# Optimization experiments

Hardware: AMD Instinct MI355X
Metric: run time of the kernel (lower is better)

## Reference

```python
import jax, jax.numpy as jnp
import numpy as np

B, N, C, H = 2, 2048, 1024, 16
D = C // H  # head_dim = 64

def setup_inputs() -> dict:
    key = jax.random.key(0)
    ks = jax.random.split(key, 8)
    x = jax.random.normal(ks[0], (B, N, C), jnp.float32)
    mask = jax.random.uniform(ks[1], (H, N, N), jnp.float32)
    gamma = jax.random.uniform(ks[2], (H,), jnp.float32)  # per-head decay in (0,1)
    state_prev = jax.random.normal(ks[3], (B, H, D, D), jnp.float32)
    w_scale = 0.02
    W_qkv = jax.random.normal(ks[4], (C, 3 * C), jnp.float32) * w_scale
    b_qkv = jnp.zeros((3 * C,), jnp.float32)
    W_out = jax.random.normal(ks[5], (C, C), jnp.float32) * w_scale
    b_out = jnp.zeros((C,), jnp.float32)
    return dict(x=x, mask=mask, gamma=gamma, state_prev=state_prev,
                W_qkv=W_qkv, b_qkv=b_qkv, W_out=W_out, b_out=b_out)

def reference(x, mask, gamma, state_prev, W_qkv, b_qkv, W_out, b_out):
    # Retention.chunkwise with state_prev (mode='chunkwise')
    b, n, c = x.shape
    h = gamma.shape[0]
    d = c // h
    scale = d ** -0.5
    qkv = (x @ W_qkv + b_qkv).reshape(b, n, 3, h, d)
    q = qkv[:, :, 0].transpose(0, 2, 1, 3) * scale  # [B,H,N,D]
    k = qkv[:, :, 1].transpose(0, 2, 1, 3)
    v = qkv[:, :, 2].transpose(0, 2, 1, 3)
    # intra-chunk decay-masked retention: [B,H,N,N]
    ret = jnp.einsum('bhnd,bhmd->bhnm', q, k) * mask
    ret = jnp.einsum('bhnm,bhmd->bhnd', ret, v)  # [B,H,N,D]
    inner_pos = jnp.arange(1, n + 1, dtype=x.dtype)  # [N], 1-based positions
    # state = sum_n gamma^(N-n) * k_n^T v_n (no [B,H,N,D,D] materialization)
    state_decays = gamma[:, None] ** (n - inner_pos)[None, :]  # [H,N]
    state = jnp.einsum('bhnd,bhne,hn->bhde', k, v, state_decays)  # [B,H,D,D]
    chunk_decay = gamma ** n  # [H]
    state = state + state_prev * chunk_decay[None, :, None, None]
    # cross-chunk retention against previous state
    cross = jnp.einsum('bhnd,bhde->bhne', q, state_prev)
    cross = cross * (gamma[None, :, None, None] ** inner_pos[None, None, :, None])
    ret = (ret + cross).transpose(0, 2, 1, 3).reshape(b, n, c)
    out = ret @ W_out + b_out
    return (out, state)
```

## Files before the change

kernel.cpp:

```cpp
#include <hip/hip_runtime.h>
#include <hip/hip_bf16.h>
#include <cstdint>

#define DI __device__ __forceinline__

typedef __attribute__((ext_vector_type(8))) short v8s;
typedef __attribute__((ext_vector_type(4))) float v4f;

constexpr int Bc = 2, Nc = 2048, Cc = 1024, Hc = 16, Dc = 64;

DI float bfbits(uint32_t u) { union { uint32_t i; float f; } c; c.i = u; return c.f; }
DI unsigned short f2bf(float f) {
    union { float f; uint32_t u; } c; c.f = f;
    uint32_t r = c.u + 0x7FFFu + ((c.u >> 16) & 1u);
    return (unsigned short)(r >> 16);
}
DI void unpackb8(uint4 u, float* f) {
    f[0] = bfbits(u.x << 16); f[1] = bfbits(u.x & 0xFFFF0000u);
    f[2] = bfbits(u.y << 16); f[3] = bfbits(u.y & 0xFFFF0000u);
    f[4] = bfbits(u.z << 16); f[5] = bfbits(u.z & 0xFFFF0000u);
    f[6] = bfbits(u.w << 16); f[7] = bfbits(u.w & 0xFFFF0000u);
}
DI float gpow(float g, float p) {
    if (p <= 0.f) return 1.f;
    if (g <= 0.f) return 0.f;
    return exp2f(p * log2f(g));
}

__global__ __launch_bounds__(256) void cvt_bf16(
    const float* __restrict__ in, unsigned short* __restrict__ out, int n8)
{
    int i = blockIdx.x * 256 + threadIdx.x;
    if (i >= n8) return;
    float4 a = ((const float4*)in)[i * 2];
    float4 b = ((const float4*)in)[i * 2 + 1];
    ushort4 r0; r0.x = f2bf(a.x); r0.y = f2bf(a.y); r0.z = f2bf(a.z); r0.w = f2bf(a.w);
    ushort4 r1; r1.x = f2bf(b.x); r1.y = f2bf(b.y); r1.z = f2bf(b.z); r1.w = f2bf(b.w);
    ((ushort4*)out)[i * 2] = r0; ((ushort4*)out)[i * 2 + 1] = r1;
}

__global__ __launch_bounds__(256) void transpose_cvt(
    const float* __restrict__ in, unsigned short* __restrict__ out, int R, int C)
{
    __shared__ float T[64][65];
    const int tid = threadIdx.x;
    const int r0 = blockIdx.y * 64, c0 = blockIdx.x * 64;
    #pragma unroll
    for (int rep = 0; rep < 4; rep++) {
        int row = (tid >> 4) + rep * 16, col = (tid & 15) * 4;
        float4 v = *reinterpret_cast<const float4*>(in + (size_t)(r0 + row) * C + c0 + col);
        T[row][col] = v.x; T[row][col + 1] = v.y; T[row][col + 2] = v.z; T[row][col + 3] = v.w;
    }
    __syncthreads();
    #pragma unroll
    for (int rep = 0; rep < 4; rep++) {
        int ocr = (tid >> 4) + rep * 16, j4 = (tid & 15) * 4;
        ushort4 w;
        w.x = f2bf(T[j4][ocr]);     w.y = f2bf(T[j4 + 1][ocr]);
        w.z = f2bf(T[j4 + 2][ocr]); w.w = f2bf(T[j4 + 3][ocr]);
        *reinterpret_cast<ushort4*>(out + (size_t)(c0 + ocr) * R + r0 + j4) = w;
    }
}

__global__ __launch_bounds__(256) void qkv_mfma(
    const unsigned short* __restrict__ A, const unsigned short* __restrict__ Bt,
    const float* __restrict__ bias,
    unsigned short* __restrict__ q, unsigned short* __restrict__ k,
    unsigned short* __restrict__ v)
{
    __shared__ unsigned short As[128][72];
    __shared__ unsigned short Bs[128][72];
    const int tid = threadIdx.x, wave = tid >> 6, lane = tid & 63;
    const int L = lane & 15, quad = lane >> 4;
    const int wr = (wave >> 1) * 64, wc = (wave & 1) * 64;
    const int row0 = blockIdx.y * 128, col0 = blockIdx.x * 128;
    v4f acc[4][4];
    #pragma unroll
    for (int i = 0; i < 4; i++)
        #pragma unroll
        for (int j = 0; j < 4; j++) { acc[i][j][0]=0.f; acc[i][j][1]=0.f; acc[i][j][2]=0.f; acc[i][j][3]=0.f; }
    for (int k0 = 0; k0 < 1024; k0 += 64) {
        __syncthreads();
        #pragma unroll
        for (int rep = 0; rep < 4; rep++) {
            int r = (tid >> 3) + rep * 32, cg = (tid & 7) * 8;
            *(uint4*)&As[r][cg] = *(const uint4*)(A  + (size_t)(row0 + r) * 1024 + k0 + cg);
            *(uint4*)&Bs[r][cg] = *(const uint4*)(Bt + (size_t)(col0 + r) * 1024 + k0 + cg);
        }
        __syncthreads();
        #pragma unroll
        for (int half = 0; half < 2; half++) {
            v8s af[4], bf[4];
            #pragma unroll
            for (int s = 0; s < 4; s++) {
                af[s] = *(v8s*)&As[wr + s * 16 + L][half * 32 + quad * 8];
                bf[s] = *(v8s*)&Bs[wc + s * 16 + L][half * 32 + quad * 8];
            }
            #pragma unroll
            for (int i = 0; i < 4; i++)
                #pragma unroll
                for (int j = 0; j < 4; j++)
                    acc[i][j] = __builtin_amdgcn_mfma_f32_16x16x32_bf16(af[i], bf[j], acc[i][j], 0, 0, 0);
        }
    }
    const int which = col0 >> 10;
    #pragma unroll
    for (int j = 0; j < 4; j++) {
        int c = col0 + wc + j * 16 + L;
        int h = (c & 1023) >> 6, d = c & 63;
        float bv = bias[c];
        #pragma unroll
        for (int i = 0; i < 4; i++) {
            #pragma unroll
            for (int reg = 0; reg < 4; reg++) {
                int rr = row0 + wr + i * 16 + quad * 4 + reg;
                int b = rr >> 11, n = rr & 2047;
                float val = acc[i][j][reg] + bv;
                size_t base = (((size_t)(b * Hc + h)) * Nc + n) * Dc + d;
                if (which == 0)      q[base] = f2bf(val * 0.125f);
                else if (which == 1) k[base] = f2bf(val);
                else                 v[base] = f2bf(val);
            }
        }
    }
}

__global__ __launch_bounds__(256) void retention_mfma(
    const unsigned short* __restrict__ qb, const unsigned short* __restrict__ kb,
    const unsigned short* __restrict__ vb,
    const float* __restrict__ mask, const float* __restrict__ gamma,
    const float* __restrict__ sprev,
    unsigned short* __restrict__ retb)
{
    __shared__ unsigned short K0[64][72], K1[64][72];
    __shared__ unsigned short V0[64][72], V1[64][72];
    __shared__ unsigned short Sm[64][72];
    const int tid = threadIdx.x, wave = tid >> 6, lane = tid & 63;
    const int L = lane & 15, quad = lane >> 4;
    const int h = blockIdx.y;
    const int n0 = blockIdx.x * 64;
    const float g = gamma[h];
    const int bh0 = h, bh1 = Hc + h;

    {
        #pragma unroll
        for (int rep = 0; rep < 2; rep++) {
            int r = (tid >> 3) + rep * 32, ch = (tid & 7) * 8;
            *(uint4*)&V0[r][ch] = *(const uint4*)(qb + ((size_t)bh0 * Nc + n0 + r) * Dc + ch);
            *(uint4*)&V1[r][ch] = *(const uint4*)(qb + ((size_t)bh1 * Nc + n0 + r) * Dc + ch);
        }
        int dd = tid >> 2, e0 = (tid & 3) * 16;
        const float* sp0 = sprev + ((size_t)bh0 * 64 + dd) * 64 + e0;
        const float* sp1 = sprev + ((size_t)bh1 * 64 + dd) * 64 + e0;
        #pragma unroll
        for (int j = 0; j < 16; j++) K0[e0 + j][dd] = f2bf(sp0[j]);
        #pragma unroll
        for (int j = 0; j < 16; j++) K1[e0 + j][dd] = f2bf(sp1[j]);
    }
    __syncthreads();
    v8s qf[2][2];
    qf[0][0] = *(v8s*)&V0[wave * 16 + L][quad * 8];
    qf[0][1] = *(v8s*)&V0[wave * 16 + L][32 + quad * 8];
    qf[1][0] = *(v8s*)&V1[wave * 16 + L][quad * 8];
    qf[1][1] = *(v8s*)&V1[wave * 16 + L][32 + quad * 8];
    v4f oacc[2][4];
    #pragma unroll
    for (int b = 0; b < 2; b++) {
        unsigned short (*Kb)[72] = b ? K1 : K0;
        #pragma unroll
        for (int s = 0; s < 4; s++) {
            v4f a; a[0] = 0.f; a[1] = 0.f; a[2] = 0.f; a[3] = 0.f;
            a = __builtin_amdgcn_mfma_f32_16x16x32_bf16(qf[b][0], *(v8s*)&Kb[s * 16 + L][quad * 8], a, 0, 0, 0);
            a = __builtin_amdgcn_mfma_f32_16x16x32_bf16(qf[b][1], *(v8s*)&Kb[s * 16 + L][32 + quad * 8], a, 0, 0, 0);
            oacc[b][s] = a;
        }
    }
    {
        float cf = gpow(g, (float)(n0 + wave * 16 + quad * 4 + 1));
        #pragma unroll
        for (int reg = 0; reg < 4; reg++) {
            #pragma unroll
            for (int b = 0; b < 2; b++)
                #pragma unroll
                for (int s = 0; s < 4; s++) oacc[b][s][reg] *= cf;
            cf *= g;
        }
    }

    const float* mbase = mask + (size_t)h * Nc * Nc;
    const unsigned short* kp0 = kb + (size_t)bh0 * Nc * Dc;
    const unsigned short* kp1 = kb + (size_t)bh1 * Nc * Dc;
    const unsigned short* vp0 = vb + (size_t)bh0 * Nc * Dc;
    const unsigned short* vp1 = vb + (size_t)bh1 * Nc * Dc;

    for (int m0 = 0; m0 < Nc; m0 += 64) {
        __syncthreads();
        {
            #pragma unroll
            for (int rep = 0; rep < 2; rep++) {
                int r = (tid >> 3) + rep * 32, ch = (tid & 7) * 8;
                *(uint4*)&K0[r][ch] = *(const uint4*)(kp0 + (size_t)(m0 + r) * Dc + ch);
                *(uint4*)&K1[r][ch] = *(const uint4*)(kp1 + (size_t)(m0 + r) * Dc + ch);
            }
            int n = tid >> 2, d0 = (tid & 3) * 16;
            union { uint4 u[2]; unsigned short s[16]; } tv;
            tv.u[0] = *(const uint4*)(vp0 + (size_t)(m0 + n) * Dc + d0);
            tv.u[1] = *(const uint4*)(vp0 + (size_t)(m0 + n) * Dc + d0 + 8);
            #pragma unroll
            for (int j = 0; j < 16; j++) V0[d0 + j][n] = tv.s[j];
            tv.u[0] = *(const uint4*)(vp1 + (size_t)(m0 + n) * Dc + d0);
            tv.u[1] = *(const uint4*)(vp1 + (size_t)(m0 + n) * Dc + d0 + 8);
            #pragma unroll
            for (int j = 0; j < 16; j++) V1[d0 + j][n] = tv.s[j];
        }
        __syncthreads();
        float mv[4][4];
        #pragma unroll
        for (int s = 0; s < 4; s++)
            #pragma unroll
            for (int reg = 0; reg < 4; reg++)
                mv[s][reg] = mbase[(size_t)(n0 + wave * 16 + quad * 4 + reg) * Nc + m0 + s * 16 + L];
        #pragma unroll
        for (int b = 0; b < 2; b++) {
            unsigned short (*Kb)[72] = b ? K1 : K0;
            unsigned short (*Vb)[72] = b ? V1 : V0;
            v4f sa[4];
            #pragma unroll
            for (int s = 0; s < 4; s++) {
                v4f a; a[0] = 0.f; a[1] = 0.f; a[2] = 0.f; a[3] = 0.f;
                a = __builtin_amdgcn_mfma_f32_16x16x32_bf16(qf[b][0], *(v8s*)&Kb[s * 16 + L][quad * 8], a, 0, 0, 0);
                a = __builtin_amdgcn_mfma_f32_16x16x32_bf16(qf[b][1], *(v8s*)&Kb[s * 16 + L][32 + quad * 8], a, 0, 0, 0);
                sa[s] = a;
            }
            #pragma unroll
            for (int s = 0; s < 4; s++)
                #pragma unroll
                for (int reg = 0; reg < 4; reg++)
                    Sm[wave * 16 + quad * 4 + reg][s * 16 + L] = f2bf(sa[s][reg] * mv[s][reg]);
            v8s af0 = *(v8s*)&Sm[wave * 16 + L][quad * 8];
            v8s af1 = *(v8s*)&Sm[wave * 16 + L][32 + quad * 8];
            #pragma unroll
            for (int s = 0; s < 4; s++) {
                oacc[b][s] = __builtin_amdgcn_mfma_f32_16x16x32_bf16(af0, *(v8s*)&Vb[s * 16 + L][quad * 8], oacc[b][s], 0, 0, 0);
                oacc[b][s] = __builtin_amdgcn_mfma_f32_16x16x32_bf16(af1, *(v8s*)&Vb[s * 16 + L][32 + quad * 8], oacc[b][s], 0, 0, 0);
            }
        }
    }
    #pragma unroll
    for (int b = 0; b < 2; b++)
        #pragma unroll
        for (int s = 0; s < 4; s++)
            #pragma unroll
            for (int reg = 0; reg < 4; reg++) {
                int n = n0 + wave * 16 + quad * 4 + reg;
                retb[((size_t)b * Nc + n) * Cc + h * 64 + s * 16 + L] = f2bf(oacc[b][s][reg]);
            }
}

__global__ __launch_bounds__(256) void state_partial(
    const unsigned short* __restrict__ kg, const unsigned short* __restrict__ vg,
    const float* __restrict__ gamma,
    float* __restrict__ partial)
{
    __shared__ float Ks[64][65];
    __shared__ float Vs[64][65];
    __shared__ float wdec[64];
    const int chunk = blockIdx.x;
    const int bh = blockIdx.y;
    const int h = bh & 15;
    const int tid = threadIdx.x;
    const int d = tid >> 2;
    const int e0 = (tid & 3) * 16;
    const float g = gamma[h];
    const unsigned short* kbp = kg + (size_t)bh * Nc * Dc;
    const unsigned short* vbp = vg + (size_t)bh * Nc * Dc;
    float acc[16] = {};
    const int nStart = chunk * 256;
    for (int m0 = nStart; m0 < nStart + 256; m0 += 64) {
        __syncthreads();
        {
            uint4 u0 = *(const uint4*)(kbp + (size_t)(m0 + d) * 64 + e0);
            uint4 u1 = *(const uint4*)(kbp + (size_t)(m0 + d) * 64 + e0 + 8);
            float f[8];
            unpackb8(u0, f);
            #pragma unroll
            for (int j = 0; j < 8; j++) Ks[d][e0 + j] = f[j];
            unpackb8(u1, f);
            #pragma unroll
            for (int j = 0; j < 8; j++) Ks[d][e0 + 8 + j] = f[j];
            uint4 w0 = *(const uint4*)(vbp + (size_t)(m0 + d) * 64 + e0);
            uint4 w1 = *(const uint4*)(vbp + (size_t)(m0 + d) * 64 + e0 + 8);
            unpackb8(w0, f);
            #pragma unroll
            for (int j = 0; j < 8; j++) Vs[d][e0 + j] = f[j];
            unpackb8(w1, f);
            #pragma unroll
            for (int j = 0; j < 8; j++) Vs[d][e0 + 8 + j] = f[j];
        }
        if (tid < 64) wdec[tid] = gpow(g, (float)(2047 - (m0 + tid)));
        __syncthreads();
        for (int nn = 0; nn < 64; nn++) {
            float kw = Ks[nn][d] * wdec[nn];
            #pragma unroll
            for (int j = 0; j < 16; j++) acc[j] += kw * Vs[nn][e0 + j];
        }
    }
    float* pp = partial + (size_t)chunk * (Bc * Hc * Dc * Dc)
              + ((size_t)bh * 64 + d) * 64 + e0;
    #pragma unroll
    for (int j = 0; j < 16; j++) pp[j] = acc[j];
}

__global__ __launch_bounds__(256) void state_reduce(
    const float* __restrict__ partial,
    const float* __restrict__ sprev,
    const float* __restrict__ gamma,
    float* __restrict__ outState)
{
    const int idx = blockIdx.x * 256 + threadIdx.x;
    const int bh = idx >> 12;
    const int h = bh & 15;
    const float g = gamma[h];
    float acc = sprev[idx] * gpow(g, 2048.f);
    #pragma unroll
    for (int c = 0; c < 8; c++) acc += partial[(size_t)c * (Bc * Hc * Dc * Dc) + idx];
    outState[idx] = acc;
}

__global__ __launch_bounds__(256) void out_mfma(
    const unsigned short* __restrict__ A, const unsigned short* __restrict__ Bt,
    const float* __restrict__ bias,
    float* __restrict__ out)
{
    __shared__ unsigned short As[128][72];
    __shared__ unsigned short Bs[128][72];
    const int tid = threadIdx.x, wave = tid >> 6, lane = tid & 63;
    const int L = lane & 15, quad = lane >> 4;
    const int wr = (wave >> 1) * 64, wc = (wave & 1) * 64;
    const int row0 = blockIdx.y * 128, col0 = blockIdx.x * 128;
    v4f acc[4][4];
    #pragma unroll
    for (int i = 0; i < 4; i++)
        #pragma unroll
        for (int j = 0; j < 4; j++) { acc[i][j][0]=0.f; acc[i][j][1]=0.f; acc[i][j][2]=0.f; acc[i][j][3]=0.f; }
    for (int k0 = 0; k0 < 1024; k0 += 64) {
        __syncthreads();
        #pragma unroll
        for (int rep = 0; rep < 4; rep++) {
            int r = (tid >> 3) + rep * 32, cg = (tid & 7) * 8;
            *(uint4*)&As[r][cg] = *(const uint4*)(A  + (size_t)(row0 + r) * 1024 + k0 + cg);
            *(uint4*)&Bs[r][cg] = *(const uint4*)(Bt + (size_t)(col0 + r) * 1024 + k0 + cg);
        }
        __syncthreads();
        #pragma unroll
        for (int half = 0; half < 2; half++) {
            v8s af[4], bf[4];
            #pragma unroll
            for (int s = 0; s < 4; s++) {
                af[s] = *(v8s*)&As[wr + s * 16 + L][half * 32 + quad * 8];
                bf[s] = *(v8s*)&Bs[wc + s * 16 + L][half * 32 + quad * 8];
            }
            #pragma unroll
            for (int i = 0; i < 4; i++)
                #pragma unroll
                for (int j = 0; j < 4; j++)
                    acc[i][j] = __builtin_amdgcn_mfma_f32_16x16x32_bf16(af[i], bf[j], acc[i][j], 0, 0, 0);
        }
    }
    #pragma unroll
    for (int j = 0; j < 4; j++) {
        int c = col0 + wc + j * 16 + L;
        float bv = bias[c];
        #pragma unroll
        for (int i = 0; i < 4; i++) {
            #pragma unroll
            for (int reg = 0; reg < 4; reg++) {
                int rr = row0 + wr + i * 16 + quad * 4 + reg;
                out[(size_t)rr * 1024 + c] = acc[i][j][reg] + bv;
            }
        }
    }
}

extern "C" void kernel_launch(void* const* d_in, const int* in_sizes, int n_in,
                              void* d_out, int out_size, void* d_ws, size_t ws_size,
                              hipStream_t stream) {
    (void)in_sizes; (void)n_in; (void)out_size; (void)ws_size;
    const float* x     = (const float*)d_in[0];
    const float* mask  = (const float*)d_in[1];
    const float* gamma = (const float*)d_in[2];
    const float* sprev = (const float*)d_in[3];
    const float* Wqkv  = (const float*)d_in[4];
    const float* bqkv  = (const float*)d_in[5];
    const float* Wout  = (const float*)d_in[6];
    const float* bout  = (const float*)d_in[7];

    char* W = (char*)d_ws;
    unsigned short* qb   = (unsigned short*)(W);
    unsigned short* kb   = (unsigned short*)(W + 8388608);
    unsigned short* vb   = (unsigned short*)(W + 16777216);
    unsigned short* retb = (unsigned short*)(W + 33554432);
    unsigned short* xb   = (unsigned short*)(W + 41943040);
    unsigned short* wqt  = (unsigned short*)(W + 50331648);
    unsigned short* wot  = (unsigned short*)(W + 56623104);
    float*          part = (float*)        (W + 58720256);

    float* out      = (float*)d_out;
    float* outState = (float*)d_out + (size_t)Bc * Nc * Cc;

    cvt_bf16<<<2048, 256, 0, stream>>>(x, xb, 524288);
    transpose_cvt<<<dim3(48, 16), 256, 0, stream>>>(Wqkv, wqt, 1024, 3072);
    transpose_cvt<<<dim3(16, 16), 256, 0, stream>>>(Wout, wot, 1024, 1024);
    qkv_mfma<<<dim3(24, 32), 256, 0, stream>>>(xb, wqt, bqkv, qb, kb, vb);
    retention_mfma<<<dim3(32, 16), 256, 0, stream>>>(qb, kb, vb, mask, gamma, sprev, retb);
    state_partial<<<dim3(8, 32), 256, 0, stream>>>(kb, vb, gamma, part);
    state_reduce<<<512, 256, 0, stream>>>(part, sprev, gamma, outState);
    out_mfma<<<dim3(8, 32), 256, 0, stream>>>(retb, wot, bout, out);
}
```

Measured before the change: 574.5 us.

## Split retention over key chunks, pre-transpose V, and prefetch tiles in registers

Splits the retention kernel's key dimension into two chunks via a third grid dimension, doubling block count from 512 to 1024. The second chunk writes fp32 partials that a new add_partial kernel folds into the bf16 output. V is transposed once by a separate kernel so tile loads become plain vector copies, and the next K/V/mask tile is prefetched into registers while the current one is computed. The cost is extra fp32 partial traffic, another launch, an extra bf16 rounding, and workspace buffers reused across phases.

```diff
diff --git a/kernel.cpp b/kernel.cpp
--- a/kernel.cpp
+++ b/kernel.cpp
@@ -59,6 +59,31 @@
         w.x = f2bf(T[j4][ocr]);     w.y = f2bf(T[j4 + 1][ocr]);
         w.z = f2bf(T[j4 + 2][ocr]); w.w = f2bf(T[j4 + 3][ocr]);
         *reinterpret_cast<ushort4*>(out + (size_t)(c0 + ocr) * R + r0 + j4) = w;
+    }
+}
+
+__global__ __launch_bounds__(256) void transpose_v(
+    const unsigned short* __restrict__ in, unsigned short* __restrict__ out)
+{
+    __shared__ unsigned short T[64][72];
+    const int tid = threadIdx.x;
+    const int n0 = blockIdx.x * 64;
+    const int bh = blockIdx.y;
+    const unsigned short* src = in + ((size_t)bh * Nc + n0) * Dc;
+    #pragma unroll
+    for (int rep = 0; rep < 2; rep++) {
+        int r = (tid >> 3) + rep * 32, c = (tid & 7) * 8;
+        *(uint4*)&T[r][c] = *(const uint4*)(src + (size_t)r * Dc + c);
+    }
+    __syncthreads();
+    unsigned short* dst = out + (size_t)bh * Dc * Nc + n0;
+    #pragma unroll
+    for (int rep = 0; rep < 2; rep++) {
+        int d = (tid >> 3) + rep * 32, c0 = (tid & 7) * 8;
+        union { uint4 u; unsigned short s[8]; } w;
+        #pragma unroll
+        for (int j = 0; j < 8; j++) w.s[j] = T[c0 + j][d];
+        *(uint4*)(dst + (size_t)d * Nc + c0) = w.u;
     }
 }
 
@@ -125,12 +150,12 @@
     }
 }
 
-__global__ __launch_bounds__(256) void retention_mfma(
+__global__ __launch_bounds__(256, 3) void retention_mfma(
     const unsigned short* __restrict__ qb, const unsigned short* __restrict__ kb,
-    const unsigned short* __restrict__ vb,
+    const unsigned short* __restrict__ vtb,
     const float* __restrict__ mask, const float* __restrict__ gamma,
     const float* __restrict__ sprev,
-    unsigned short* __restrict__ retb)
+    unsigned short* __restrict__ retb, float* __restrict__ pf0, float* __restrict__ pf1)
 {
     __shared__ unsigned short K0[64][72], K1[64][72];
     __shared__ unsigned short V0[64][72], V1[64][72];
@@ -139,6 +164,8 @@
     const int L = lane & 15, quad = lane >> 4;
     const int h = blockIdx.y;
     const int n0 = blockIdx.x * 64;
+    const int chunk = blockIdx.z;
+    const int m_base = chunk * 1024;
     const float g = gamma[h];
     const int bh0 = h, bh1 = Hc + h;
 
@@ -149,13 +176,15 @@
             *(uint4*)&V0[r][ch] = *(const uint4*)(qb + ((size_t)bh0 * Nc + n0 + r) * Dc + ch);
             *(uint4*)&V1[r][ch] = *(const uint4*)(qb + ((size_t)bh1 * Nc + n0 + r) * Dc + ch);
         }
-        int dd = tid >> 2, e0 = (tid & 3) * 16;
-        const float* sp0 = sprev + ((size_t)bh0 * 64 + dd) * 64 + e0;
-        const float* sp1 = sprev + ((size_t)bh1 * 64 + dd) * 64 + e0;
-        #pragma unroll
-        for (int j = 0; j < 16; j++) K0[e0 + j][dd] = f2bf(sp0[j]);
-        #pragma unroll
-        for (int j = 0; j < 16; j++) K1[e0 + j][dd] = f2bf(sp1[j]);
+        if (chunk == 0) {
+            int dd = tid >> 2, e0 = (tid & 3) * 16;
+            const float* sp0 = sprev + ((size_t)bh0 * 64 + dd) * 64 + e0;
+            const float* sp1 = sprev + ((size_t)bh1 * 64 + dd) * 64 + e0;
+            #pragma unroll
+            for (int j = 0; j < 16; j++) K0[e0 + j][dd] = f2bf(sp0[j]);
+            #pragma unroll
+            for (int j = 0; j < 16; j++) K1[e0 + j][dd] = f2bf(sp1[j]);
+        }
     }
     __syncthreads();
     v8s qf[2][2];
@@ -164,18 +193,18 @@
     qf[1][0] = *(v8s*)&V1[wave * 16 + L][quad * 8];
     qf[1][1] = *(v8s*)&V1[wave * 16 + L][32 + quad * 8];
     v4f oacc[2][4];
-    #pragma unroll
-    for (int b = 0; b < 2; b++) {
-        unsigned short (*Kb)[72] = b ? K1 : K0;
-        #pragma unroll
-        for (int s = 0; s < 4; s++) {
-            v4f a; a[0] = 0.f; a[1] = 0.f; a[2] = 0.f; a[3] = 0.f;
-            a = __builtin_amdgcn_mfma_f32_16x16x32_bf16(qf[b][0], *(v8s*)&Kb[s * 16 + L][quad * 8], a, 0, 0, 0);
-            a = __builtin_amdgcn_mfma_f32_16x16x32_bf16(qf[b][1], *(v8s*)&Kb[s * 16 + L][32 + quad * 8], a, 0, 0, 0);
-            oacc[b][s] = a;
-        }
-    }
-    {
+    if (chunk == 0) {
+        #pragma unroll
+        for (int b = 0; b < 2; b++) {
+            unsigned short (*Kb)[72] = b ? K1 : K0;
+            #pragma unroll
+            for (int s = 0; s < 4; s++) {
+                v4f a; a[0] = 0.f; a[1] = 0.f; a[2] = 0.f; a[3] = 0.f;
+                a = __builtin_amdgcn_mfma_f32_16x16x32_bf16(qf[b][0], *(v8s*)&Kb[s * 16 + L][quad * 8], a, 0, 0, 0);
+                a = __builtin_amdgcn_mfma_f32_16x16x32_bf16(qf[b][1], *(v8s*)&Kb[s * 16 + L][32 + quad * 8], a, 0, 0, 0);
+                oacc[b][s] = a;
+            }
+        }
         float cf = gpow(g, (float)(n0 + wave * 16 + quad * 4 + 1));
         #pragma unroll
         for (int reg = 0; reg < 4; reg++) {
@@ -185,41 +214,72 @@
                 for (int s = 0; s < 4; s++) oacc[b][s][reg] *= cf;
             cf *= g;
         }
-    }
-
-    const float* mbase = mask + (size_t)h * Nc * Nc;
+    } else {
+        #pragma unroll
+        for (int b = 0; b < 2; b++)
+            #pragma unroll
+            for (int s = 0; s < 4; s++) { oacc[b][s][0]=0.f; oacc[b][s][1]=0.f; oacc[b][s][2]=0.f; oacc[b][s][3]=0.f; }
+    }
+
     const unsigned short* kp0 = kb + (size_t)bh0 * Nc * Dc;
     const unsigned short* kp1 = kb + (size_t)bh1 * Nc * Dc;
-    const unsigned short* vp0 = vb + (size_t)bh0 * Nc * Dc;
-    const unsigned short* vp1 = vb + (size_t)bh1 * Nc * Dc;
-
-    for (int m0 = 0; m0 < Nc; m0 += 64) {
-        __syncthreads();
-        {
+    const unsigned short* vt0 = vtb + (size_t)bh0 * Dc * Nc;
+    const unsigned short* vt1 = vtb + (size_t)bh1 * Dc * Nc;
+    const float* mptr = mask + (size_t)h * Nc * Nc
+                      + (size_t)(n0 + wave * 16 + quad * 4) * Nc + L;
+
+    const int r1 = tid >> 3, ch = (tid & 7) * 8;
+    uint4 pk0[2], pk1[2], pv0[2], pv1[2];
+    float mv[4][4];
+    {
+        const int m0 = m_base;
+        #pragma unroll
+        for (int rep = 0; rep < 2; rep++) {
+            int r = r1 + rep * 32;
+            pk0[rep] = *(const uint4*)(kp0 + (size_t)(m0 + r) * Dc + ch);
+            pk1[rep] = *(const uint4*)(kp1 + (size_t)(m0 + r) * Dc + ch);
+            pv0[rep] = *(const uint4*)(vt0 + (size_t)r * Nc + m0 + ch);
+            pv1[rep] = *(const uint4*)(vt1 + (size_t)r * Nc + m0 + ch);
+        }
+        #pragma unroll
+        for (int s = 0; s < 4; s++)
+            #pragma unroll
+            for (int reg = 0; reg < 4; reg++)
+                mv[s][reg] = mptr[(size_t)reg * Nc + m0 + s * 16];
+    }
+
+    for (int it = 0; it < 16; ++it) {
+        __syncthreads();
+        #pragma unroll
+        for (int rep = 0; rep < 2; rep++) {
+            int r = r1 + rep * 32;
+            *(uint4*)&K0[r][ch] = pk0[rep];
+            *(uint4*)&K1[r][ch] = pk1[rep];
+            *(uint4*)&V0[r][ch] = pv0[rep];
+            *(uint4*)&V1[r][ch] = pv1[rep];
+        }
+        float mc[4][4];
+        #pragma unroll
+        for (int s = 0; s < 4; s++)
+            #pragma unroll
+            for (int reg = 0; reg < 4; reg++) mc[s][reg] = mv[s][reg];
+        __syncthreads();
+        if (it < 15) {
+            const int m0 = m_base + (it + 1) * 64;
             #pragma unroll
             for (int rep = 0; rep < 2; rep++) {
-                int r = (tid >> 3) + rep * 32, ch = (tid & 7) * 8;
-                *(uint4*)&K0[r][ch] = *(const uint4*)(kp0 + (size_t)(m0 + r) * Dc + ch);
-                *(uint4*)&K1[r][ch] = *(const uint4*)(kp1 + (size_t)(m0 + r) * Dc + ch);
-            }
-            int n = tid >> 2, d0 = (tid & 3) * 16;
-            union { uint4 u[2]; unsigned short s[16]; } tv;
-            tv.u[0] = *(const uint4*)(vp0 + (size_t)(m0 + n) * Dc + d0);
-            tv.u[1] = *(const uint4*)(vp0 + (size_t)(m0 + n) * Dc + d0 + 8);
-            #pragma unroll
-            for (int j = 0; j < 16; j++) V0[d0 + j][n] = tv.s[j];
-            tv.u[0] = *(const uint4*)(vp1 + (size_t)(m0 + n) * Dc + d0);
-            tv.u[1] = *(const uint4*)(vp1 + (size_t)(m0 + n) * Dc + d0 + 8);
-            #pragma unroll
-            for (int j = 0; j < 16; j++) V1[d0 + j][n] = tv.s[j];
-        }
-        __syncthreads();
-        float mv[4][4];
-        #pragma unroll
-        for (int s = 0; s < 4; s++)
-            #pragma unroll
-            for (int reg = 0; reg < 4; reg++)
-                mv[s][reg] = mbase[(size_t)(n0 + wave * 16 + quad * 4 + reg) * Nc + m0 + s * 16 + L];
+                int r = r1 + rep * 32;
+                pk0[rep] = *(const uint4*)(kp0 + (size_t)(m0 + r) * Dc + ch);
+                pk1[rep] = *(const uint4*)(kp1 + (size_t)(m0 + r) * Dc + ch);
+                pv0[rep] = *(const uint4*)(vt0 + (size_t)r * Nc + m0 + ch);
+                pv1[rep] = *(const uint4*)(vt1 + (size_t)r * Nc + m0 + ch);
+            }
+            #pragma unroll
+            for (int s = 0; s < 4; s++)
+                #pragma unroll
+                for (int reg = 0; reg < 4; reg++)
+                    mv[s][reg] = mptr[(size_t)reg * Nc + m0 + s * 16];
+        }
         #pragma unroll
         for (int b = 0; b < 2; b++) {
             unsigned short (*Kb)[72] = b ? K1 : K0;
@@ -236,7 +296,7 @@
             for (int s = 0; s < 4; s++)
                 #pragma unroll
                 for (int reg = 0; reg < 4; reg++)
-                    Sm[wave * 16 + quad * 4 + reg][s * 16 + L] = f2bf(sa[s][reg] * mv[s][reg]);
+                    Sm[wave * 16 + quad * 4 + reg][s * 16 + L] = f2bf(sa[s][reg] * mc[s][reg]);
             v8s af0 = *(v8s*)&Sm[wave * 16 + L][quad * 8];
             v8s af1 = *(v8s*)&Sm[wave * 16 + L][32 + quad * 8];
             #pragma unroll
@@ -246,15 +306,49 @@
             }
         }
     }
-    #pragma unroll
-    for (int b = 0; b < 2; b++)
-        #pragma unroll
-        for (int s = 0; s < 4; s++)
-            #pragma unroll
-            for (int reg = 0; reg < 4; reg++) {
-                int n = n0 + wave * 16 + quad * 4 + reg;
-                retb[((size_t)b * Nc + n) * Cc + h * 64 + s * 16 + L] = f2bf(oacc[b][s][reg]);
-            }
+    if (chunk == 0) {
+        #pragma unroll
+        for (int b = 0; b < 2; b++)
+            #pragma unroll
+            for (int s = 0; s < 4; s++)
+                #pragma unroll
+                for (int reg = 0; reg < 4; reg++) {
+                    int n = n0 + wave * 16 + quad * 4 + reg;
+                    retb[((size_t)b * Nc + n) * Cc + h * 64 + s * 16 + L] = f2bf(oacc[b][s][reg]);
+                }
+    } else {
+        #pragma unroll
+        for (int b = 0; b < 2; b++) {
+            float* pd = b ? pf1 : pf0;
+            #pragma unroll
+            for (int s = 0; s < 4; s++)
+                #pragma unroll
+                for (int reg = 0; reg < 4; reg++) {
+                    int n = n0 + wave * 16 + quad * 4 + reg;
+                    pd[(size_t)n * Cc + h * 64 + s * 16 + L] = oacc[b][s][reg];
+                }
+        }
+    }
+}
+
+__global__ __launch_bounds__(256) void add_partial(
+    unsigned short* __restrict__ retb,
+    const float* __restrict__ pf0, const float* __restrict__ pf1, int n8)
+{
+    int i = blockIdx.x * 256 + threadIdx.x;
+    if (i >= n8) return;
+    int e = i * 8;
+    const float* pf = (e & (1 << 21)) ? pf1 : pf0;
+    const float4* pp = (const float4*)(pf + (e & ((1 << 21) - 1)));
+    uint4 a = ((const uint4*)retb)[i];
+    float fa[8]; unpackb8(a, fa);
+    float4 x0 = pp[0], x1 = pp[1];
+    ushort4 r0, r1;
+    r0.x = f2bf(fa[0] + x0.x); r0.y = f2bf(fa[1] + x0.y);
+    r0.z = f2bf(fa[2] + x0.z); r0.w = f2bf(fa[3] + x0.w);
+    r1.x = f2bf(fa[4] + x1.x); r1.y = f2bf(fa[5] + x1.y);
+    r1.z = f2bf(fa[6] + x1.z); r1.w = f2bf(fa[7] + x1.w);
+    ((ushort4*)retb)[2 * i] = r0; ((ushort4*)retb)[2 * i + 1] = r1;
 }
 
 __global__ __launch_bounds__(256) void state_partial(
@@ -399,11 +493,14 @@
     unsigned short* qb   = (unsigned short*)(W);
     unsigned short* kb   = (unsigned short*)(W + 8388608);
     unsigned short* vb   = (unsigned short*)(W + 16777216);
-    unsigned short* retb = (unsigned short*)(W + 33554432);
-    unsigned short* xb   = (unsigned short*)(W + 41943040);
-    unsigned short* wqt  = (unsigned short*)(W + 50331648);
-    unsigned short* wot  = (unsigned short*)(W + 56623104);
-    float*          part = (float*)        (W + 58720256);
+    float*          pf0  = (float*)        (W + 16777216);
+    unsigned short* retb = (unsigned short*)(W + 25165824);
+    unsigned short* wot  = (unsigned short*)(W + 33554432);
+    float*          part = (float*)        (W + 35651584);
+    unsigned short* xb   = (unsigned short*)(W + 39845888);
+    unsigned short* vtb  = (unsigned short*)(W + 39845888);
+    unsigned short* wqt  = (unsigned short*)(W + 48234496);
+    float*          pf1  = (float*)        (W + 54525952);
 
     float* out      = (float*)d_out;
     float* outState = (float*)d_out + (size_t)Bc * Nc * Cc;
@@ -412,8 +509,11 @@
     transpose_cvt<<<dim3(48, 16), 256, 0, stream>>>(Wqkv, wqt, 1024, 3072);
     transpose_cvt<<<dim3(16, 16), 256, 0, stream>>>(Wout, wot, 1024, 1024);
     qkv_mfma<<<dim3(24, 32), 256, 0, stream>>>(xb, wqt, bqkv, qb, kb, vb);
-    retention_mfma<<<dim3(32, 16), 256, 0, stream>>>(qb, kb, vb, mask, gamma, sprev, retb);
+    transpose_v<<<dim3(32, 32), 256, 0, stream>>>(vb, vtb);
     state_partial<<<dim3(8, 32), 256, 0, stream>>>(kb, vb, gamma, part);
     state_reduce<<<512, 256, 0, stream>>>(part, sprev, gamma, outState);
+    retention_mfma<<<dim3(32, 16, 2), 256, 0, stream>>>(qb, kb, vtb, mask, gamma, sprev,
+                                                        retb, pf0, pf1);
+    add_partial<<<2048, 256, 0, stream>>>(retb, pf0, pf1, 524288);
     out_mfma<<<dim3(8, 32), 256, 0, stream>>>(retb, wot, bout, out);
 }
```

New measurement: 691.5 us. 1.2x slower.
